# Performance work log

Measured on AMD Instinct MI355X. Metric: run time of the kernel, lower is better.

The kernel has to match this reference:

```python
import jax, jax.numpy as jnp
import numpy as np

B, T, D, F, E, K = 4, 2048, 1024, 2048, 8, 2


def setup_inputs() -> dict:
    key = jax.random.key(0)
    ks = jax.random.split(key, 5)
    s = lambda n: 1.0 / np.sqrt(n)
    return {
        "x": jax.random.normal(ks[0], (B, T, D), jnp.float32),
        "gate_w": jax.random.normal(ks[1], (D, E), jnp.float32) * s(D),
        "gate_b": jnp.zeros((E,), jnp.float32),
        "w1": jax.random.normal(ks[2], (E, D, F), jnp.float32) * s(D),
        "b1": jnp.zeros((E, F), jnp.float32),
        "w2": jax.random.normal(ks[3], (E, F, D), jnp.float32) * s(F),
        "b2": jnp.zeros((E, D), jnp.float32),
    }


def reference(x, gate_w, gate_b, w1, b1, w2, b2):
    # Router: gate logits -> top-k -> softmax over the k selected logits
    logits = x @ gate_w + gate_b                      # [B,T,E]
    top_v, top_i = jax.lax.top_k(logits, K)           # [B,T,K]
    top_w = jax.nn.softmax(top_v, axis=-1)            # [B,T,K]
    # Dense combine weights per expert: w_full[b,t,e] = sum_k top_w * 1[top_i==e]
    one_hot = jax.nn.one_hot(top_i, E, dtype=x.dtype)  # [B,T,K,E]
    w_full = jnp.sum(top_w[..., None] * one_hot, axis=-2)  # [B,T,E]
    # All-experts FFN (batched over expert dim), exact-erf GELU as in nn.GELU()
    h = jax.nn.gelu(jnp.einsum('btd,edf->ebtf', x, w1) + b1[:, None, None, :],
                    approximate=False)                 # [E,B,T,F]
    y = jnp.einsum('ebtf,efd->ebtd', h, w2) + b2[:, None, None, :]  # [E,B,T,D]
    # Weighted combine (zero weight for unselected experts == masked dispatch)
    return jnp.einsum('bte,ebtd->btd', w_full, y)      # [B,T,D]
```

## Files before the change

### kernel.cpp

```cpp
#include <hip/hip_runtime.h>
#include <hip/hip_bf16.h>
#include <math.h>

#define B_ 4
#define T_ 2048
#define D_ 1024
#define F_ 2048
#define E_ 8
#define NT (B_ * T_)
#define NS (NT * 2)
#define CAP (NS + E_ * 128)

typedef __attribute__((ext_vector_type(8))) short short8;
typedef __attribute__((ext_vector_type(4))) float floatx4;

static __device__ __forceinline__ unsigned short f2bf(float f) {
  union { float f; unsigned u; } a; a.f = f;
  unsigned r = a.u + 0x7fffu + ((a.u >> 16) & 1u);
  return (unsigned short)(r >> 16);
}

static __device__ __forceinline__ float bf2f(unsigned u) {
  union { unsigned u; float f; } a; a.u = u << 16; return a.f;
}

static __device__ __forceinline__ void gld16(const unsigned short* g, unsigned short* l) {
  __builtin_amdgcn_global_load_lds(
      (const __attribute__((address_space(1))) void*)g,
      (__attribute__((address_space(3))) void*)l, 16, 0, 0);
}

static __device__ __forceinline__ float gelu_f(float v) {
  float ax = fabsf(v) * 0.70710678118654752f;
  float t = __builtin_amdgcn_rcpf(1.f + 0.3275911f * ax);
  float e = __builtin_amdgcn_exp2f(-ax * ax * 1.44269504088896f);
  float p = t * (0.254829592f +
            t * (-0.284496736f +
            t * (1.421413741f +
            t * (-1.453152027f +
            t * 1.061405429f))));
  float er = 1.f - p * e;
  er = copysignf(er, v);
  return 0.5f * v * (1.f + er);
}

__global__ void transpose_cvt(const float* __restrict__ in, unsigned short* __restrict__ out,
                              int R, int C) {
  __shared__ float tile[64][65];
  int e = blockIdx.z;
  const float* inp = in + (size_t)e * R * C;
  unsigned short* outp = out + (size_t)e * R * C;
  int c0 = blockIdx.x * 64, r0 = blockIdx.y * 64;
  int tid = threadIdx.x;
  int rl = tid >> 4;
  int cl = (tid & 15) * 4;
#pragma unroll
  for (int jr = 0; jr < 4; jr++) {
    int row = rl + 16 * jr;
    float4 v = *(const float4*)&inp[(size_t)(r0 + row) * C + c0 + cl];
    tile[row][cl + 0] = v.x; tile[row][cl + 1] = v.y;
    tile[row][cl + 2] = v.z; tile[row][cl + 3] = v.w;
  }
  __syncthreads();
  int cc0 = tid >> 3;
  int rq = (tid & 7) * 8;
#pragma unroll
  for (int jc = 0; jc < 2; jc++) {
    int cc = cc0 + 32 * jc;
    unsigned w[4];
#pragma unroll
    for (int i = 0; i < 4; i++) {
      unsigned lo = f2bf(tile[rq + 2 * i][cc]);
      unsigned hi = f2bf(tile[rq + 2 * i + 1][cc]);
      w[i] = lo | (hi << 16);
    }
    *(uint4*)&outp[(size_t)(c0 + cc) * R + r0 + rq] = make_uint4(w[0], w[1], w[2], w[3]);
  }
}

__global__ void router_k(const float* __restrict__ x, const float* __restrict__ gw,
                         const float* __restrict__ gb, int* __restrict__ ti,
                         float* __restrict__ tw) {
  int wid = threadIdx.x >> 6, lane = threadIdx.x & 63;
  int t = blockIdx.x * 4 + wid;
  const float* xr = x + (size_t)t * D_;
  float acc[E_];
#pragma unroll
  for (int e = 0; e < E_; e++) acc[e] = 0.f;
#pragma unroll
  for (int it = 0; it < D_ / 64; it++) {
    int d = it * 64 + lane;
    float xv = xr[d];
    const float* g = gw + d * E_;
#pragma unroll
    for (int e = 0; e < E_; e++) acc[e] += xv * g[e];
  }
#pragma unroll
  for (int off = 32; off > 0; off >>= 1)
#pragma unroll
    for (int e = 0; e < E_; e++) acc[e] += __shfl_xor(acc[e], off);
  if (lane == 0) {
    float v[E_];
#pragma unroll
    for (int e = 0; e < E_; e++) v[e] = acc[e] + gb[e];
    int i0 = 0; float v0 = v[0];
#pragma unroll
    for (int e = 1; e < E_; e++) if (v[e] > v0) { v0 = v[e]; i0 = e; }
    int i1 = -1; float v1 = -3.4e38f;
#pragma unroll
    for (int e = 0; e < E_; e++) if (e != i0 && v[e] > v1) { v1 = v[e]; i1 = e; }
    float ex = expf(v1 - v0);
    float w0 = 1.f / (1.f + ex);
    float w1 = ex / (1.f + ex);
    ti[2 * t] = i0; tw[2 * t] = w0;
    ti[2 * t + 1] = i1; tw[2 * t + 1] = w1;
  }
}

__global__ void count_prefix_k(const int* __restrict__ ti, int* __restrict__ offs,
                               int* __restrict__ cursors) {
  __shared__ int scnt[4][E_];
  int tid = threadIdx.x;
  int cnt[E_];
#pragma unroll
  for (int k = 0; k < E_; k++) cnt[k] = 0;
  for (int i = tid; i < NS; i += 256) {
    int e = ti[i];
#pragma unroll
    for (int k = 0; k < E_; k++) cnt[k] += (e == k) ? 1 : 0;
  }
#pragma unroll
  for (int off = 32; off > 0; off >>= 1)
#pragma unroll
    for (int k = 0; k < E_; k++) cnt[k] += __shfl_xor(cnt[k], off);
  int wid = tid >> 6, lane = tid & 63;
  if (lane == 0)
#pragma unroll
    for (int k = 0; k < E_; k++) scnt[wid][k] = cnt[k];
  __syncthreads();
  if (tid == 0) {
    int o = 0;
    for (int k = 0; k < E_; k++) {
      int c = scnt[0][k] + scnt[1][k] + scnt[2][k] + scnt[3][k];
      offs[k] = o;
      cursors[k] = o;
      o += (c + 127) & ~127;
    }
    offs[E_] = o;
  }
}

__global__ void scatter_k(const int* __restrict__ ti, const float* __restrict__ tw,
                          int* __restrict__ cursors, int* __restrict__ idx,
                          int* __restrict__ pos_of) {
  int a = blockIdx.x * 256 + threadIdx.x;
  int lane = threadIdx.x & 63;
  int e = ti[a];
  unsigned long long m[E_];
#pragma unroll
  for (int k = 0; k < E_; k++) m[k] = __ballot(e == k);
  int base = 0;
  if (lane < E_) base = atomicAdd(&cursors[lane], __popcll(m[lane]));
  int myBase = __shfl(base, e);
  unsigned long long m_mine = 0;
#pragma unroll
  for (int k = 0; k < E_; k++) if (e == k) m_mine = m[k];
  int rank = __popcll(m_mine & ((1ull << lane) - 1ull));
  int pos = myBase + rank;
  idx[pos] = a >> 1;
  pos_of[a] = pos;
}

__global__ void gather_k(const float* __restrict__ x, const int* __restrict__ idx,
                         unsigned short* __restrict__ Xg) {
  int s = blockIdx.x;
  int t = idx[s];
  t = ((unsigned)t < (unsigned)NT) ? t : 0;
  const float4* xr = (const float4*)(x + (size_t)t * D_);
  float4 v = xr[threadIdx.x];
  uint2 p;
  p.x = (unsigned)f2bf(v.x) | ((unsigned)f2bf(v.y) << 16);
  p.y = (unsigned)f2bf(v.z) | ((unsigned)f2bf(v.w) << 16);
  ((uint2*)(Xg + (size_t)s * D_))[threadIdx.x] = p;
}

template <int K, int N, bool GELU>
__global__ __launch_bounds__(256, 3) void gemm_k(const unsigned short* __restrict__ A,
                                                 const unsigned short* __restrict__ W,
                                                 const float* __restrict__ bias_all,
                                                 unsigned short* __restrict__ O,
                                                 const int* __restrict__ offs) {
  constexpr int NC = N / 128;
  int h = blockIdx.x;
  int logical = (h & 7) * ((int)gridDim.x >> 3) + (h >> 3);
  int rt = logical / NC, ct = logical - rt * NC;
  int slot0 = rt * 128;
  if (slot0 >= offs[E_]) return;
  int e = 0;
  while (slot0 >= offs[e + 1]) e++;
  const unsigned short* Bp = W + (size_t)e * N * K;
  int n0 = ct * 128;

  __shared__ unsigned short lA[3][128 * 32];
  __shared__ unsigned short lB[3][128 * 32];

  int tid = threadIdx.x;
  int wid = tid >> 6, lane = tid & 63;
  int wr = wid >> 1, wc = wid & 1;
  int quad = lane >> 4, l15 = lane & 15;

  int cph = (((l15 & 1) << 2) | quad) ^ ((l15 >> 1) & 7);
  int ra = ((wr << 5) + (l15 >> 1)) * 64 + cph * 8;
  int rb = ((wc << 5) + (l15 >> 1)) * 64 + cph * 8;

  int srl = lane >> 3;
  int clog = (lane & 7) ^ srl;
  int r_l = (srl << 1) | (clog >> 2);
  int q_l = clog & 3;
  const unsigned short* gA = A + (size_t)(slot0 + 32 * wid + r_l) * K + q_l * 8;
  const unsigned short* gB = Bp + (size_t)(n0 + 32 * wid + r_l) * K + q_l * 8;

#define STG(buf, kt) do {                                                \
    gld16(gA + (size_t)(kt) * 32, &lA[buf][(32 * wid) * 32]);            \
    gld16(gA + (size_t)16 * K + (size_t)(kt) * 32,                       \
          &lA[buf][(32 * wid + 16) * 32]);                               \
    gld16(gB + (size_t)(kt) * 32, &lB[buf][(32 * wid) * 32]);            \
    gld16(gB + (size_t)16 * K + (size_t)(kt) * 32,                       \
          &lB[buf][(32 * wid + 16) * 32]);                               \
  } while (0)
#define SYNC4 asm volatile("s_waitcnt vmcnt(4)\n\ts_barrier" ::: "memory")

  floatx4 acc[4][4];
#pragma unroll
  for (int mi = 0; mi < 4; mi++)
#pragma unroll
    for (int ni = 0; ni < 4; ni++) acc[mi][ni] = (floatx4){0.f, 0.f, 0.f, 0.f};

  constexpr int NK = K / 32;

  STG(0, 0);
  STG(1, 1);
  SYNC4;

#define STEP(j, t) do {                                                  \
    int kt = ((t) + 2 < NK) ? (t) + 2 : 0;                               \
    STG(((j) + 2) % 3, kt);                                              \
    short8 af[4], bfr[4];                                                \
    _Pragma("unroll")                                                    \
    for (int m = 0; m < 4; m++) af[m] = *(const short8*)&lA[j][ra + m * 512]; \
    _Pragma("unroll")                                                    \
    for (int n = 0; n < 4; n++) bfr[n] = *(const short8*)&lB[j][rb + n * 512]; \
    _Pragma("unroll")                                                    \
    for (int m = 0; m < 4; m++)                                          \
      _Pragma("unroll")                                                  \
      for (int n = 0; n < 4; n++)                                        \
        acc[m][n] = __builtin_amdgcn_mfma_f32_16x16x32_bf16(af[m], bfr[n], acc[m][n], 0, 0, 0); \
    SYNC4;                                                               \
  } while (0)

  for (int t3 = 0; t3 < NK; t3 += 3) {
    STEP(0, t3);
    if (t3 + 1 < NK) STEP(1, t3 + 1);
    if (t3 + 2 < NK) STEP(2, t3 + 2);
  }
#undef STEP
#undef STG
#undef SYNC4

  const float* bias = bias_all + (size_t)e * N;
#pragma unroll
  for (int mi = 0; mi < 4; mi++) {
    int row = slot0 + 64 * wr + 16 * mi + quad * 4;
#pragma unroll
    for (int ni = 0; ni < 4; ni++) {
      int col = n0 + 64 * wc + 16 * ni + l15;
      float bv = bias[col];
#pragma unroll
      for (int r = 0; r < 4; r++) {
        float v = acc[mi][ni][r] + bv;
        if (GELU) v = gelu_f(v);
        O[(size_t)(row + r) * N + col] = f2bf(v);
      }
    }
  }
}

__global__ void combine_k(const unsigned short* __restrict__ Yg,
                          const int* __restrict__ pos_of,
                          const float* __restrict__ tw, float* __restrict__ out) {
  int t = blockIdx.x;
  int p0 = pos_of[2 * t], p1 = pos_of[2 * t + 1];
  float w0 = tw[2 * t], w1 = tw[2 * t + 1];
  uint2 a = ((const uint2*)(Yg + (size_t)p0 * D_))[threadIdx.x];
  uint2 b = ((const uint2*)(Yg + (size_t)p1 * D_))[threadIdx.x];
  float4 r;
  r.x = w0 * bf2f(a.x & 0xffffu) + w1 * bf2f(b.x & 0xffffu);
  r.y = w0 * bf2f(a.x >> 16)     + w1 * bf2f(b.x >> 16);
  r.z = w0 * bf2f(a.y & 0xffffu) + w1 * bf2f(b.y & 0xffffu);
  r.w = w0 * bf2f(a.y >> 16)     + w1 * bf2f(b.y >> 16);
  ((float4*)(out + (size_t)t * D_))[threadIdx.x] = r;
}

extern "C" void kernel_launch(void* const* d_in, const int* in_sizes, int n_in,
                              void* d_out, int out_size, void* d_ws, size_t ws_size,
                              hipStream_t stream) {
  const float* x  = (const float*)d_in[0];
  const float* gw = (const float*)d_in[1];
  const float* gb = (const float*)d_in[2];
  const float* w1 = (const float*)d_in[3];
  const float* b1 = (const float*)d_in[4];
  const float* w2 = (const float*)d_in[5];
  const float* b2 = (const float*)d_in[6];
  float* out = (float*)d_out;

  char* p = (char*)d_ws;
  unsigned short* w1t = (unsigned short*)p; p += (size_t)E_ * D_ * F_ * 2;
  unsigned short* w2t = (unsigned short*)p; p += (size_t)E_ * D_ * F_ * 2;
  unsigned short* Xg  = (unsigned short*)p; p += (size_t)CAP * D_ * 2;
  unsigned short* H   = (unsigned short*)p; p += (size_t)CAP * F_ * 2;
  int*   idx    = (int*)p; p += (size_t)CAP * 4;
  int*   pos_of = (int*)p; p += (size_t)NS * 4;
  int*   ti     = (int*)p; p += (size_t)NS * 4;
  float* tw     = (float*)p; p += (size_t)NS * 4;
  int* cursors = (int*)p; p += 64;
  int* offs    = (int*)p; p += 64;
  unsigned short* Yg = Xg;

  transpose_cvt<<<dim3(F_ / 64, D_ / 64, E_), 256, 0, stream>>>(w1, w1t, D_, F_);
  transpose_cvt<<<dim3(D_ / 64, F_ / 64, E_), 256, 0, stream>>>(w2, w2t, F_, D_);
  router_k<<<NT / 4, 256, 0, stream>>>(x, gw, gb, ti, tw);
  count_prefix_k<<<1, 256, 0, stream>>>(ti, offs, cursors);
  scatter_k<<<NS / 256, 256, 0, stream>>>(ti, tw, cursors, idx, pos_of);
  gather_k<<<CAP, 256, 0, stream>>>(x, idx, Xg);
  gemm_k<D_, F_, true><<<dim3((CAP / 128) * (F_ / 128)), 256, 0, stream>>>(Xg, w1t, b1, H, offs);
  gemm_k<F_, D_, false><<<dim3((CAP / 128) * (D_ / 128)), 256, 0, stream>>>(H, w2t, b2, Yg, offs);
  combine_k<<<NT, 256, 0, stream>>>(Yg, pos_of, tw, out);
}
```

Before: 465.0 us.

## Pre-swizzle weights into MFMA fragment layout and load B directly to registers

```diff
diff --git a/kernel.cpp b/kernel.cpp
--- a/kernel.cpp
+++ b/kernel.cpp
@@ -44,13 +44,18 @@
   return 0.5f * v * (1.f + er);
 }
 
-__global__ void transpose_cvt(const float* __restrict__ in, unsigned short* __restrict__ out,
-                              int R, int C) {
+__global__ void transpose_cvt(const float* __restrict__ w1, const float* __restrict__ w2,
+                              unsigned short* __restrict__ w1t, unsigned short* __restrict__ w2t) {
   __shared__ float tile[64][65];
-  int e = blockIdx.z;
-  const float* inp = in + (size_t)e * R * C;
-  unsigned short* outp = out + (size_t)e * R * C;
-  int c0 = blockIdx.x * 64, r0 = blockIdx.y * 64;
+  int id = blockIdx.x;
+  bool second = id >= 512;
+  int lid = second ? id - 512 : id;
+  int R = second ? F_ : D_, C = second ? D_ : F_;
+  int nx = C / 64;
+  int ty = lid / nx, tx = lid - ty * nx;
+  const float* inp = (second ? w2 : w1) + (size_t)blockIdx.y * R * C;
+  unsigned short* outp = (second ? w2t : w1t) + (size_t)blockIdx.y * R * C;
+  int c0 = tx * 64, r0 = ty * 64;
   int tid = threadIdx.x;
   int rl = tid >> 4;
   int cl = (tid & 15) * 4;
@@ -74,7 +79,11 @@
       unsigned hi = f2bf(tile[rq + 2 * i + 1][cc]);
       w[i] = lo | (hi << 16);
     }
-    *(uint4*)&outp[(size_t)(c0 + cc) * R + r0 + rq] = make_uint4(w[0], w[1], w[2], w[3]);
+    int n = c0 + cc, kb = r0 + rq;
+    size_t soff = (size_t)(n >> 4) * ((size_t)R << 4)
+                + (size_t)(kb >> 5) * 512
+                + (size_t)(((kb >> 3) & 3) * 16 + (n & 15)) * 8;
+    *(uint4*)&outp[soff] = make_uint4(w[0], w[1], w[2], w[3]);
   }
 }
 
@@ -191,6 +200,7 @@
                                                  unsigned short* __restrict__ O,
                                                  const int* __restrict__ offs) {
   constexpr int NC = N / 128;
+  constexpr int NK = K / 32;
   int h = blockIdx.x;
   int logical = (h & 7) * ((int)gridDim.x >> 3) + (h >> 3);
   int rt = logical / NC, ct = logical - rt * NC;
@@ -198,11 +208,10 @@
   if (slot0 >= offs[E_]) return;
   int e = 0;
   while (slot0 >= offs[e + 1]) e++;
-  const unsigned short* Bp = W + (size_t)e * N * K;
+  const unsigned short* gWp = W + (size_t)e * N * K;
   int n0 = ct * 128;
 
-  __shared__ unsigned short lA[3][128 * 32];
-  __shared__ unsigned short lB[3][128 * 32];
+  __shared__ unsigned short lA[4][128 * 32];
 
   int tid = threadIdx.x;
   int wid = tid >> 6, lane = tid & 63;
@@ -211,61 +220,62 @@
 
   int cph = (((l15 & 1) << 2) | quad) ^ ((l15 >> 1) & 7);
   int ra = ((wr << 5) + (l15 >> 1)) * 64 + cph * 8;
-  int rb = ((wc << 5) + (l15 >> 1)) * 64 + cph * 8;
 
   int srl = lane >> 3;
   int clog = (lane & 7) ^ srl;
   int r_l = (srl << 1) | (clog >> 2);
   int q_l = clog & 3;
   const unsigned short* gA = A + (size_t)(slot0 + 32 * wid + r_l) * K + q_l * 8;
-  const unsigned short* gB = Bp + (size_t)(n0 + 32 * wid + r_l) * K + q_l * 8;
-
-#define STG(buf, kt) do {                                                \
+
+  int n16b = (n0 >> 4) + (wc << 2);
+
+  short8 bq0[4], bq1[4];
+  floatx4 acc[4][4];
+#pragma unroll
+  for (int mi = 0; mi < 4; mi++)
+#pragma unroll
+    for (int ni = 0; ni < 4; ni++) acc[mi][ni] = (floatx4){0.f, 0.f, 0.f, 0.f};
+
+#define STGA(buf, kt) do {                                               \
     gld16(gA + (size_t)(kt) * 32, &lA[buf][(32 * wid) * 32]);            \
     gld16(gA + (size_t)16 * K + (size_t)(kt) * 32,                       \
           &lA[buf][(32 * wid + 16) * 32]);                               \
-    gld16(gB + (size_t)(kt) * 32, &lB[buf][(32 * wid) * 32]);            \
-    gld16(gB + (size_t)16 * K + (size_t)(kt) * 32,                       \
-          &lB[buf][(32 * wid + 16) * 32]);                               \
   } while (0)
-#define SYNC4 asm volatile("s_waitcnt vmcnt(4)\n\ts_barrier" ::: "memory")
-
-  floatx4 acc[4][4];
-#pragma unroll
-  for (int mi = 0; mi < 4; mi++)
-#pragma unroll
-    for (int ni = 0; ni < 4; ni++) acc[mi][ni] = (floatx4){0.f, 0.f, 0.f, 0.f};
-
-  constexpr int NK = K / 32;
-
-  STG(0, 0);
-  STG(1, 1);
-  SYNC4;
-
-#define STEP(j, t) do {                                                  \
+#define LOADB(dst, tt)                                                    \
+    _Pragma("unroll")                                                     \
+    for (int n_ = 0; n_ < 4; n_++)                                        \
+      dst[n_] = *(const short8*)&gWp[((size_t)(n16b + n_) * NK + (tt)) * 512 + lane * 8]
+
+  STGA(0, 0);
+  LOADB(bq0, 0);
+  STGA(1, 1);
+  asm volatile("s_waitcnt vmcnt(2)\n\ts_barrier" ::: "memory");
+
+#define STEP(j, t, BR, BW) do {                                          \
+    int bt = ((t) + 1 < NK) ? (t) + 1 : 0;   \
     int kt = ((t) + 2 < NK) ? (t) + 2 : 0;                               \
-    STG(((j) + 2) % 3, kt);                                              \
-    short8 af[4], bfr[4];                                                \
+    LOADB(BW, bt);                                                       \
+    STGA((j + 2) & 3, kt);                                               \
+    short8 af[4];                                                        \
     _Pragma("unroll")                                                    \
     for (int m = 0; m < 4; m++) af[m] = *(const short8*)&lA[j][ra + m * 512]; \
     _Pragma("unroll")                                                    \
-    for (int n = 0; n < 4; n++) bfr[n] = *(const short8*)&lB[j][rb + n * 512]; \
-    _Pragma("unroll")                                                    \
     for (int m = 0; m < 4; m++)                                          \
       _Pragma("unroll")                                                  \
-      for (int n = 0; n < 4; n++)                                        \
-        acc[m][n] = __builtin_amdgcn_mfma_f32_16x16x32_bf16(af[m], bfr[n], acc[m][n], 0, 0, 0); \
-    SYNC4;                                                               \
+      for (int n_ = 0; n_ < 4; n_++)                                     \
+        acc[m][n_] = __builtin_amdgcn_mfma_f32_16x16x32_bf16(af[m], BR[n_], acc[m][n_], 0, 0, 0); \
+    asm volatile("s_waitcnt vmcnt(2)\n\ts_barrier" ::: "memory");        \
   } while (0)
 
-  for (int t3 = 0; t3 < NK; t3 += 3) {
-    STEP(0, t3);
-    if (t3 + 1 < NK) STEP(1, t3 + 1);
-    if (t3 + 2 < NK) STEP(2, t3 + 2);
+  for (int t4 = 0; t4 < NK; t4 += 4) {
+    STEP(0, t4,     bq0, bq1);
+    STEP(1, t4 + 1, bq1, bq0);
+    STEP(2, t4 + 2, bq0, bq1);
+    STEP(3, t4 + 3, bq1, bq0);
   }
 #undef STEP
-#undef STG
-#undef SYNC4
+#undef STGA
+#undef LOADB
 
   const float* bias = bias_all + (size_t)e * N;
 #pragma unroll
@@ -326,8 +336,7 @@
   int* offs    = (int*)p; p += 64;
   unsigned short* Yg = Xg;
 
-  transpose_cvt<<<dim3(F_ / 64, D_ / 64, E_), 256, 0, stream>>>(w1, w1t, D_, F_);
-  transpose_cvt<<<dim3(D_ / 64, F_ / 64, E_), 256, 0, stream>>>(w2, w2t, F_, D_);
+  transpose_cvt<<<dim3(1024, E_), 256, 0, stream>>>(w1, w2, w1t, w2t);
   router_k<<<NT / 4, 256, 0, stream>>>(x, gw, gb, ti, tw);
   count_prefix_k<<<1, 256, 0, stream>>>(ti, offs, cursors);
   scatter_k<<<NS / 256, 256, 0, stream>>>(ti, tw, cursors, idx, pos_of);
```

Result: no change. 458.6 us (-1.4%).
